# Kernel tuning notes

Measured on AMD Instinct MI355X. Metric: run time of the kernel, lower is better.

Reference implementation:

```python
import jax, jax.numpy as jnp
import numpy as np

# B videos, K topological sorts, N subtask nodes, S video segments, H = hsize
B, K, N, S, H = 8, 4, 16, 64, 512
NEG = -100.0  # torch.full((N,S), -100.0) init in dp_align


def setup_inputs() -> dict:
    key = jax.random.key(0)
    ks = jax.random.split(key, 6)
    return {
        "seg_text_feats": jax.random.normal(ks[0], (B, K, N, 2 * H), jnp.float32),
        "vid_feature": jax.random.normal(ks[1], (B, S, 2 * H), jnp.float32),
        "labels": jax.random.uniform(ks[2], (B,), jnp.float32),
        "W1": jax.random.normal(ks[3], (4 * H, H), jnp.float32) * 0.02,
        "b1": jnp.zeros((H,), jnp.float32),
        "w2": jax.random.normal(ks[4], (H,), jnp.float32) * 0.04,
        "b2": jnp.zeros((), jnp.float32),
    }


def _dp_single(logits):
    """Viterbi-style banded DP of dp_align for one (video, sort) pair.
    logits: [N, S]. Returns (best_score=arr[0,0], aggregated_logits, alignment[N]).
    Recurrence (faithful to the torch code):
      arr[n,s] = max(V_curr, arr[n,s+1]) where
        V_curr = logsig(logit[n,s])                     if n == N-1
        V_curr = logsig(logit[n,s]) + arr[n+1, s]       otherwise
      band: s in [n, S-N+n]; out-of-band cells stay -100.
    """
    n_nodes, n_segs = logits.shape
    L = jax.nn.log_sigmoid(logits)
    s_idx = jnp.arange(n_segs)

    def row_step(arr_next, xn):
        n, Ln = xn
        c = jnp.where(n == n_nodes - 1, Ln, Ln + arr_next)  # V_opt_curr per segment
        in_band = (s_idx >= n) & (s_idx <= n_segs - n_nodes + n)
        # arr[n,s] = max(max_{s'>=s in band} c[s'], -100)  (reverse cummax == seg loop)
        cm = jax.lax.cummax(jnp.where(in_band, c, -jnp.inf)[::-1])[::-1]
        row = jnp.where(in_band, jnp.maximum(cm, NEG), NEG)
        # choice[s]: took V_opt_curr (ties -> curr, matching >=); base case s=S-1 forced curr
        row_nxt = jnp.concatenate([row[1:], jnp.full((1,), -1e30, row.dtype)])
        choice = in_band & (c >= row_nxt)
        return row, (row, choice)

    arr0 = jnp.full((n_segs,), NEG, logits.dtype)
    xs = (jnp.arange(n_nodes - 1, -1, -1), L[::-1])  # nodes processed bottom-up
    _, (rows, choices) = jax.lax.scan(row_step, arr0, xs)
    best = rows[-1][0]          # arr[0, 0]
    choice = choices[::-1]      # reorder to ascending node index

    # Backpointer traceback: curr -> (node+1, seg+1) (record seg), next -> (node, seg+1)
    def step(state, _):
        node, seg, done, agg, align = state
        took = (~done) & choice[node, seg]
        agg = agg + jnp.where(took, logits[node, seg], 0.0)
        align = align.at[node].set(jnp.where(took, seg, align[node]))
        done = done | (took & (node == n_nodes - 1))
        node = jnp.where(took & (~done), node + 1, node)
        seg = jnp.where(done, seg, jnp.minimum(seg + 1, n_segs - 1))
        return (node, seg, done, agg, align), None

    init = (jnp.int32(0), jnp.int32(0), jnp.bool_(False),
            jnp.zeros((), logits.dtype), jnp.zeros((n_nodes,), jnp.int32))
    (_, _, _, agg, align), _ = jax.lax.scan(step, init, None, length=n_nodes + n_segs)
    return best, agg, align


def reference(seg_text_feats, vid_feature, labels, W1, b1, w2, b2):
    Bx, Kx, Nx, F2 = seg_text_feats.shape
    Sx = vid_feature.shape[1]
    # Batched query MLP over all (sort, node, segment) pairs (replaces the per-pair
    # batch-1 Linear+ReLU+Linear launches in the torch loop). Dropout(0.5) is eval-mode identity.
    t = jnp.broadcast_to(seg_text_feats[:, :, :, None, :], (Bx, Kx, Nx, Sx, F2))
    v = jnp.broadcast_to(vid_feature[:, None, None, :, :], (Bx, Kx, Nx, Sx, F2))
    cat = jnp.concatenate([t, v], axis=-1)                      # [B,K,N,S,4H]
    h1 = jax.nn.relu(jnp.einsum('bknsf,fh->bknsh', cat, W1) + b1)
    logits = jnp.einsum('bknsh,h->bkns', h1, w2) + b2           # [B,K,N,S]

    best, agg, align = jax.vmap(jax.vmap(_dp_single))(logits)   # [B,K], [B,K], [B,K,N]
    k = jnp.argmax(best, axis=-1)                               # best sort per video
    agg_b = jnp.take_along_axis(agg, k[:, None], axis=1)[:, 0]
    align_b = jnp.take_along_axis(align, k[:, None, None], axis=1)[:, 0]
    probs = jax.nn.sigmoid(agg_b)                               # ent_probs, [B]
    return probs, labels, align_b
```

## Files before the change

kernel.cpp:

```cpp
#include <hip/hip_runtime.h>
#include <math.h>

#define Bsz 8
#define Kc 4
#define Nn 16
#define Ss 64
#define Hh 512
#define F2 1024

__device__ __forceinline__ float logsigf(float x) {
    return fminf(x, 0.0f) - log1pf(expf(-fabsf(x)));
}

template<int Ctrl, int RowMask>
__device__ __forceinline__ float dpp_add(float x) {
    int v = __builtin_amdgcn_update_dpp(0, __float_as_int(x), Ctrl, RowMask, 0xf, false);
    return x + __int_as_float(v);
}
template<int Ctrl, int RowMask>
__device__ __forceinline__ float dpp_max(float x) {
    int v = __builtin_amdgcn_update_dpp(__float_as_int(-INFINITY), __float_as_int(x),
                                        Ctrl, RowMask, 0xf, false);
    return fmaxf(x, __int_as_float(v));
}
__device__ __forceinline__ float wave_scan_add(float x) {
    x = dpp_add<0x111, 0xf>(x);
    x = dpp_add<0x112, 0xf>(x);
    x = dpp_add<0x114, 0xf>(x);
    x = dpp_add<0x118, 0xf>(x);
    x = dpp_add<0x142, 0xa>(x);
    x = dpp_add<0x143, 0xc>(x);
    return x;
}
__device__ __forceinline__ float wave_scan_max(float x) {
    x = dpp_max<0x111, 0xf>(x);
    x = dpp_max<0x112, 0xf>(x);
    x = dpp_max<0x114, 0xf>(x);
    x = dpp_max<0x118, 0xf>(x);
    x = dpp_max<0x142, 0xa>(x);
    x = dpp_max<0x143, 0xc>(x);
    return x;
}

__global__ __launch_bounds__(512) void gemm_kernel(
    const float* __restrict__ seg, const float* __restrict__ vid,
    const float* __restrict__ W1,
    float* __restrict__ Tfin, float* __restrict__ Vfin)
{
    const int z = blockIdx.z;
    const float* __restrict__ Amat = z ? vid : seg;
    const float* __restrict__ Bmat = W1 + (z ? (size_t)F2 * Hh : 0);
    float* __restrict__ Out = z ? Vfin : Tfin;
    const int r0 = blockIdx.x * 64;
    const int n0 = blockIdx.y * 32;
    const int t = threadIdx.x;
    const int h   = t >> 8;
    const int tid = t & 255;

    __shared__ __align__(16) float As[2][2][32][68];
    __shared__ __align__(16) float Bs[2][2][32][36];

    const int mt = (tid >> 4) << 2;
    const int nt = (tid & 15) << 1;
    const int ar  = tid >> 3;
    const int ak4 = (tid & 7) << 2;
    const int bk  = tid >> 3;
    const int bc4 = (tid & 7) << 2;

    float4 ra0, ra1, rb0;
    auto load_step = [&](int s) {
        const int k0 = h * 512 + s * 32;
        ra0 = *reinterpret_cast<const float4*>(Amat + (size_t)(r0 + ar) * F2 + k0 + ak4);
        ra1 = *reinterpret_cast<const float4*>(Amat + (size_t)(r0 + ar + 32) * F2 + k0 + ak4);
        rb0 = *reinterpret_cast<const float4*>(Bmat + (size_t)(k0 + bk) * Hh + n0 + bc4);
    };
    auto write_step = [&](int buf) {
        As[h][buf][ak4 + 0][ar] = ra0.x; As[h][buf][ak4 + 1][ar] = ra0.y;
        As[h][buf][ak4 + 2][ar] = ra0.z; As[h][buf][ak4 + 3][ar] = ra0.w;
        As[h][buf][ak4 + 0][ar + 32] = ra1.x; As[h][buf][ak4 + 1][ar + 32] = ra1.y;
        As[h][buf][ak4 + 2][ar + 32] = ra1.z; As[h][buf][ak4 + 3][ar + 32] = ra1.w;
        *reinterpret_cast<float4*>(&Bs[h][buf][bk][bc4]) = rb0;
    };

    float acc[4][2] = {{0.f}};
    load_step(0);
    write_step(0);
    __syncthreads();
    #pragma unroll 1
    for (int s = 0; s < 16; ++s) {
        const int cur = s & 1;
        if (s + 1 < 16) load_step(s + 1);
        #pragma unroll
        for (int kk = 0; kk < 32; ++kk) {
            float4 a4 = *reinterpret_cast<const float4*>(&As[h][cur][kk][mt]);
            float2 b2 = *reinterpret_cast<const float2*>(&Bs[h][cur][kk][nt]);
            float av[4] = {a4.x, a4.y, a4.z, a4.w};
            #pragma unroll
            for (int i = 0; i < 4; ++i) {
                acc[i][0] = fmaf(av[i], b2.x, acc[i][0]);
                acc[i][1] = fmaf(av[i], b2.y, acc[i][1]);
            }
        }
        if (s + 1 < 16) {
            write_step(cur ^ 1);
            __syncthreads();
        }
    }
    __syncthreads();
    float* red = &As[0][0][0][0];
    if (h == 1) {
        #pragma unroll
        for (int i = 0; i < 4; ++i) {
            red[tid * 8 + i * 2 + 0] = acc[i][0];
            red[tid * 8 + i * 2 + 1] = acc[i][1];
        }
    }
    __syncthreads();
    if (h == 0) {
        #pragma unroll
        for (int i = 0; i < 4; ++i) {
            float2 o;
            o.x = acc[i][0] + red[tid * 8 + i * 2 + 0];
            o.y = acc[i][1] + red[tid * 8 + i * 2 + 1];
            *reinterpret_cast<float2*>(Out + (size_t)(r0 + mt + i) * Hh + n0 + nt) = o;
        }
    }
}

__global__ __launch_bounds__(256) void combine_kernel(
    const float* __restrict__ Tfin, const float* __restrict__ Vfin,
    const float* __restrict__ b1, const float* __restrict__ w2,
    const float* __restrict__ b2, float* __restrict__ logits)
{
    const int bid = blockIdx.x;
    const int b  = bid >> 5;
    const int sc = (bid >> 2) & 7;
    const int rq = bid & 3;
    const int t = threadIdx.x;
    const int wave = t >> 6, lane = t & 63;
    __shared__ float Vs[8][520];
    {
        const int s_l = t & 7;
        const int h0  = (t >> 3) << 4;
        const float* row = Vfin + (size_t)(b * Ss + sc * 8 + s_l) * Hh + h0;
        #pragma unroll
        for (int x4 = 0; x4 < 4; ++x4)
            *reinterpret_cast<float4*>(&Vs[s_l][h0 + 4 * x4]) =
                *reinterpret_cast<const float4*>(row + 4 * x4);
    }
    float w2r[8], b1r[8];
    #pragma unroll
    for (int j = 0; j < 8; ++j) { w2r[j] = w2[lane + 64 * j]; b1r[j] = b1[lane + 64 * j]; }
    const float bias2 = b2[0];
    __syncthreads();
    #pragma unroll
    for (int i = 0; i < 4; ++i) {
        const int kn = rq * 16 + wave * 4 + i;
        const int r  = b * 64 + kn;
        const float* trow = Tfin + (size_t)r * Hh;
        float tj[8];
        #pragma unroll
        for (int j = 0; j < 8; ++j) tj[j] = trow[lane + 64 * j] + b1r[j];
        #pragma unroll
        for (int s = 0; s < 8; ++s) {
            float sum = 0.f;
            #pragma unroll
            for (int j = 0; j < 8; ++j)
                sum = fmaf(fmaxf(tj[j] + Vs[s][lane + 64 * j], 0.f), w2r[j], sum);
            sum = wave_scan_add(sum);
            if (lane == 63) logits[(size_t)r * Ss + sc * 8 + s] = sum + bias2;
        }
    }
}

__global__ __launch_bounds__(256) void dp_kernel(
    const float* __restrict__ logits, const float* __restrict__ labels,
    float* __restrict__ out)
{
    const int b = blockIdx.x;
    const int t = threadIdx.x;
    const int k = t >> 6, rl = t & 63;
    const int sI = 63 - rl;
    __shared__ float lgs[Kc][Nn][Ss];
    __shared__ unsigned long long ch[Kc][Nn];
    __shared__ float bestS[Kc], aggS[Kc];
    __shared__ int alS[Kc][Nn];
    const float* lg = logits + (size_t)((b * Kc + k) * Nn) * Ss;
    float lv[Nn];
    #pragma unroll
    for (int n = 0; n < Nn; ++n) {
        lv[n] = lg[n * Ss + sI];
        lgs[k][n][sI] = lv[n];
    }
    float arr = -100.0f;
    #pragma unroll
    for (int n = Nn - 1; n >= 0; --n) {
        const float L = logsigf(lv[n]);
        const float c = (n == Nn - 1) ? L : (L + arr);
        const bool in_band = (rl <= 63 - n) && (rl >= 15 - n);
        float m = in_band ? c : -INFINITY;
        m = wave_scan_max(m);
        const float row = in_band ? fmaxf(m, -100.0f) : -100.0f;
        float rnA = __int_as_float(__builtin_amdgcn_update_dpp(
            __float_as_int(-1e30f), __float_as_int(row), 0x111, 0xf, 0xf, false));
        float b15 = __int_as_float(__builtin_amdgcn_update_dpp(
            0, __float_as_int(row), 0x142, 0xa, 0xf, false));
        float b31 = __int_as_float(__builtin_amdgcn_update_dpp(
            0, __float_as_int(row), 0x143, 0xc, 0xf, false));
        float rn = ((rl & 15) == 0 && rl != 0) ? ((rl == 32) ? b31 : b15) : rnA;
        unsigned long long mask = __ballot(in_band && (c >= rn));
        if (rl == 0) ch[k][n] = __brevll(mask);
        arr = row;
    }
    const float best = __shfl(arr, 63);
    __syncthreads();
    if (rl == 0) {
        float agg = 0.f;
        int start = 0;
        bool dead = false;
        int alignv[Nn];
        #pragma unroll
        for (int n = 0; n < Nn; ++n) {
            unsigned long long m2 = dead ? 0ull : (ch[k][n] & (~0ull << start));
            if (m2) {
                const int s = __builtin_ctzll(m2);
                agg += lgs[k][n][s];
                alignv[n] = s;
                start = s + 1;
            } else {
                alignv[n] = 0;
                dead = true;
            }
        }
        bestS[k] = best; aggS[k] = agg;
        #pragma unroll
        for (int n = 0; n < Nn; ++n) alS[k][n] = alignv[n];
    }
    __syncthreads();
    if (t == 0) {
        int kb = 0; float bb = bestS[0];
        #pragma unroll
        for (int kk = 1; kk < Kc; ++kk)
            if (bestS[kk] > bb) { bb = bestS[kk]; kb = kk; }
        out[b] = 1.0f / (1.0f + expf(-aggS[kb]));
        out[Bsz + b] = labels[b];
        #pragma unroll
        for (int n = 0; n < Nn; ++n)
            out[2 * Bsz + b * Nn + n] = (float)alS[kb][n];
    }
}

extern "C" void kernel_launch(void* const* d_in, const int* in_sizes, int n_in,
                              void* d_out, int out_size, void* d_ws, size_t ws_size,
                              hipStream_t stream) {
    const float* seg    = (const float*)d_in[0];
    const float* vid    = (const float*)d_in[1];
    const float* labels = (const float*)d_in[2];
    const float* W1     = (const float*)d_in[3];
    const float* b1     = (const float*)d_in[4];
    const float* w2     = (const float*)d_in[5];
    const float* b2     = (const float*)d_in[6];
    float* out = (float*)d_out;

    float* Tfin   = (float*)d_ws;
    float* Vfin   = Tfin + (size_t)512 * Hh;
    float* logits = Vfin + (size_t)512 * Hh;

    hipLaunchKernelGGL(gemm_kernel, dim3(8, 16, 2), dim3(512), 0, stream,
                       seg, vid, W1, Tfin, Vfin);
    hipLaunchKernelGGL(combine_kernel, dim3(256), dim3(256), 0, stream,
                       Tfin, Vfin, b1, w2, b2, logits);
    hipLaunchKernelGGL(dp_kernel, dim3(Bsz), dim3(256), 0, stream, logits, labels, out);
}
```

Baseline: 49.23 us.

## Fuse combine and DP into per-(video,sort) kernel with tiny finalize

Merges the logit-combine and Viterbi DP stages into one kernel with one block per (video, sort) pair, so logits stay in shared memory instead of going through global memory. A small finalize kernel then picks the best sort per video. The aim is to drop the global logits round trip and the DP kernel's 8-block serialization. The trade-off is that the combine work now runs on only 32 blocks instead of 256, which reduces parallelism for the heaviest stage.

```diff
diff --git a/kernel.cpp b/kernel.cpp
--- a/kernel.cpp
+++ b/kernel.cpp
@@ -127,72 +127,64 @@
     }
 }
 
-__global__ __launch_bounds__(256) void combine_kernel(
+__global__ __launch_bounds__(256) void combine_dp_kernel(
     const float* __restrict__ Tfin, const float* __restrict__ Vfin,
     const float* __restrict__ b1, const float* __restrict__ w2,
-    const float* __restrict__ b2, float* __restrict__ logits)
+    const float* __restrict__ b2, float* __restrict__ res)
 {
-    const int bid = blockIdx.x;
-    const int b  = bid >> 5;
-    const int sc = (bid >> 2) & 7;
-    const int rq = bid & 3;
+    const int blk = blockIdx.x;
+    const int b = blk >> 2;
     const int t = threadIdx.x;
     const int wave = t >> 6, lane = t & 63;
-    __shared__ float Vs[8][520];
-    {
-        const int s_l = t & 7;
-        const int h0  = (t >> 3) << 4;
-        const float* row = Vfin + (size_t)(b * Ss + sc * 8 + s_l) * Hh + h0;
-        #pragma unroll
-        for (int x4 = 0; x4 < 4; ++x4)
-            *reinterpret_cast<float4*>(&Vs[s_l][h0 + 4 * x4]) =
-                *reinterpret_cast<const float4*>(row + 4 * x4);
-    }
+    __shared__ float Vs[16][516];
+    __shared__ float lgs[Nn][Ss];
     float w2r[8], b1r[8];
     #pragma unroll
     for (int j = 0; j < 8; ++j) { w2r[j] = w2[lane + 64 * j]; b1r[j] = b1[lane + 64 * j]; }
     const float bias2 = b2[0];
-    __syncthreads();
-    #pragma unroll
-    for (int i = 0; i < 4; ++i) {
-        const int kn = rq * 16 + wave * 4 + i;
-        const int r  = b * 64 + kn;
+    float tj[4][8];
+    #pragma unroll
+    for (int n4 = 0; n4 < 4; ++n4) {
+        const int r = blk * Nn + wave * 4 + n4;
         const float* trow = Tfin + (size_t)r * Hh;
-        float tj[8];
-        #pragma unroll
-        for (int j = 0; j < 8; ++j) tj[j] = trow[lane + 64 * j] + b1r[j];
-        #pragma unroll
-        for (int s = 0; s < 8; ++s) {
-            float sum = 0.f;
+        #pragma unroll
+        for (int j = 0; j < 8; ++j) tj[n4][j] = trow[lane + 64 * j] + b1r[j];
+    }
+    #pragma unroll 1
+    for (int ch = 0; ch < 4; ++ch) {
+        __syncthreads();
+        {
+            const int s_l = t >> 4;
+            const int c0  = (t & 15) << 2;
+            const float* row = Vfin + (size_t)(b * Ss + ch * 16 + s_l) * Hh;
             #pragma unroll
-            for (int j = 0; j < 8; ++j)
-                sum = fmaf(fmaxf(tj[j] + Vs[s][lane + 64 * j], 0.f), w2r[j], sum);
-            sum = wave_scan_add(sum);
-            if (lane == 63) logits[(size_t)r * Ss + sc * 8 + s] = sum + bias2;
-        }
-    }
-}
-
-__global__ __launch_bounds__(256) void dp_kernel(
-    const float* __restrict__ logits, const float* __restrict__ labels,
-    float* __restrict__ out)
-{
-    const int b = blockIdx.x;
-    const int t = threadIdx.x;
-    const int k = t >> 6, rl = t & 63;
+            for (int x = 0; x < 8; ++x)
+                *reinterpret_cast<float4*>(&Vs[s_l][c0 + 64 * x]) =
+                    *reinterpret_cast<const float4*>(row + c0 + 64 * x);
+        }
+        __syncthreads();
+        #pragma unroll
+        for (int n4 = 0; n4 < 4; ++n4) {
+            #pragma unroll
+            for (int si = 0; si < 16; ++si) {
+                float sum = 0.f;
+                #pragma unroll
+                for (int j = 0; j < 8; ++j)
+                    sum = fmaf(fmaxf(tj[n4][j] + Vs[si][lane + 64 * j], 0.f), w2r[j], sum);
+                sum = wave_scan_add(sum);
+                if (lane == 63) lgs[wave * 4 + n4][ch * 16 + si] = sum + bias2;
+            }
+        }
+    }
+    __syncthreads();
+    if (wave != 0) return;
+    const int rl = lane;
     const int sI = 63 - rl;
-    __shared__ float lgs[Kc][Nn][Ss];
-    __shared__ unsigned long long ch[Kc][Nn];
-    __shared__ float bestS[Kc], aggS[Kc];
-    __shared__ int alS[Kc][Nn];
-    const float* lg = logits + (size_t)((b * Kc + k) * Nn) * Ss;
     float lv[Nn];
     #pragma unroll
-    for (int n = 0; n < Nn; ++n) {
-        lv[n] = lg[n * Ss + sI];
-        lgs[k][n][sI] = lv[n];
-    }
+    for (int n = 0; n < Nn; ++n) lv[n] = lgs[n][sI];
     float arr = -100.0f;
+    unsigned long long msk[Nn];
     #pragma unroll
     for (int n = Nn - 1; n >= 0; --n) {
         const float L = logsigf(lv[n]);
@@ -209,44 +201,55 @@
             0, __float_as_int(row), 0x143, 0xc, 0xf, false));
         float rn = ((rl & 15) == 0 && rl != 0) ? ((rl == 32) ? b31 : b15) : rnA;
         unsigned long long mask = __ballot(in_band && (c >= rn));
-        if (rl == 0) ch[k][n] = __brevll(mask);
+        msk[n] = __brevll(mask);
         arr = row;
     }
     const float best = __shfl(arr, 63);
-    __syncthreads();
+    float agg = 0.f;
+    int start = 0;
+    bool dead = false;
+    int alignv[Nn];
+    #pragma unroll
+    for (int n = 0; n < Nn; ++n) {
+        unsigned long long m2 = dead ? 0ull : (msk[n] & (~0ull << start));
+        if (m2) {
+            const int s = __builtin_ctzll(m2);
+            agg += __shfl(lv[n], 63 - s);
+            alignv[n] = s;
+            start = s + 1;
+        } else {
+            alignv[n] = 0;
+            dead = true;
+        }
+    }
     if (rl == 0) {
-        float agg = 0.f;
-        int start = 0;
-        bool dead = false;
-        int alignv[Nn];
-        #pragma unroll
-        for (int n = 0; n < Nn; ++n) {
-            unsigned long long m2 = dead ? 0ull : (ch[k][n] & (~0ull << start));
-            if (m2) {
-                const int s = __builtin_ctzll(m2);
-                agg += lgs[k][n][s];
-                alignv[n] = s;
-                start = s + 1;
-            } else {
-                alignv[n] = 0;
-                dead = true;
-            }
-        }
-        bestS[k] = best; aggS[k] = agg;
-        #pragma unroll
-        for (int n = 0; n < Nn; ++n) alS[k][n] = alignv[n];
-    }
-    __syncthreads();
-    if (t == 0) {
-        int kb = 0; float bb = bestS[0];
-        #pragma unroll
-        for (int kk = 1; kk < Kc; ++kk)
-            if (bestS[kk] > bb) { bb = bestS[kk]; kb = kk; }
-        out[b] = 1.0f / (1.0f + expf(-aggS[kb]));
-        out[Bsz + b] = labels[b];
+        float* rr = res + blk * 20;
+        rr[0] = best;
+        rr[1] = agg;
+        #pragma unroll
+        for (int n = 0; n < Nn; ++n) rr[2 + n] = (float)alignv[n];
+    }
+}
+
+__global__ __launch_bounds__(64) void finalize_kernel(
+    const float* __restrict__ res, const float* __restrict__ labels,
+    float* __restrict__ out)
+{
+    const int t = threadIdx.x;
+    if (t < Bsz) {
+        int kb = 0;
+        float bb = res[(t * 4 + 0) * 20];
+        #pragma unroll
+        for (int kk = 1; kk < Kc; ++kk) {
+            float v = res[(t * 4 + kk) * 20];
+            if (v > bb) { bb = v; kb = kk; }
+        }
+        const float* rr = res + (t * 4 + kb) * 20;
+        out[t] = 1.0f / (1.0f + expf(-rr[1]));
+        out[Bsz + t] = labels[t];
         #pragma unroll
         for (int n = 0; n < Nn; ++n)
-            out[2 * Bsz + b * Nn + n] = (float)alS[kb][n];
+            out[2 * Bsz + t * Nn + n] = rr[2 + n];
     }
 }
 
@@ -262,13 +265,14 @@
     const float* b2     = (const float*)d_in[6];
     float* out = (float*)d_out;
 
-    float* Tfin   = (float*)d_ws;
-    float* Vfin   = Tfin + (size_t)512 * Hh;
-    float* logits = Vfin + (size_t)512 * Hh;
+    float* Tfin = (float*)d_ws;
+    float* Vfin = Tfin + (size_t)512 * Hh;
+    float* res  = Vfin + (size_t)512 * Hh;
 
     hipLaunchKernelGGL(gemm_kernel, dim3(8, 16, 2), dim3(512), 0, stream,
                        seg, vid, W1, Tfin, Vfin);
-    hipLaunchKernelGGL(combine_kernel, dim3(256), dim3(256), 0, stream,
-                       Tfin, Vfin, b1, w2, b2, logits);
-    hipLaunchKernelGGL(dp_kernel, dim3(Bsz), dim3(256), 0, stream, logits, labels, out);
-}
+    hipLaunchKernelGGL(combine_dp_kernel, dim3(32), dim3(256), 0, stream,
+                       Tfin, Vfin, b1, w2, b2, res);
+    hipLaunchKernelGGL(finalize_kernel, dim3(1), dim3(64), 0, stream,
+                       res, labels, out);
+}
```

Result: slower. 71.46 us (+45.1%).

## Split GEMM K across four groups with 4x4 register tiles; widen combine grid

Applied to the files above, without the earlier changes.

The GEMM now uses four 128-thread groups, each covering a quarter of K with a 4x4 register tile per thread instead of a 4x2 tile, and reduces the partial sums through shared memory. The aim is more FMAs per shared-memory load and fewer serial K steps per block. The combine kernel doubles its grid, gives each wave two rows that share every V load, and uses coalesced V staging, which adds parallelism and reuse. The cost is a larger shared-memory footprint and a heavier three-way reduction at the end of the GEMM.

```diff
diff --git a/kernel.cpp b/kernel.cpp
--- a/kernel.cpp
+++ b/kernel.cpp
@@ -24,21 +24,15 @@
     return fmaxf(x, __int_as_float(v));
 }
 __device__ __forceinline__ float wave_scan_add(float x) {
-    x = dpp_add<0x111, 0xf>(x);
-    x = dpp_add<0x112, 0xf>(x);
-    x = dpp_add<0x114, 0xf>(x);
-    x = dpp_add<0x118, 0xf>(x);
-    x = dpp_add<0x142, 0xa>(x);
-    x = dpp_add<0x143, 0xc>(x);
+    x = dpp_add<0x111, 0xf>(x); x = dpp_add<0x112, 0xf>(x);
+    x = dpp_add<0x114, 0xf>(x); x = dpp_add<0x118, 0xf>(x);
+    x = dpp_add<0x142, 0xa>(x); x = dpp_add<0x143, 0xc>(x);
     return x;
 }
 __device__ __forceinline__ float wave_scan_max(float x) {
-    x = dpp_max<0x111, 0xf>(x);
-    x = dpp_max<0x112, 0xf>(x);
-    x = dpp_max<0x114, 0xf>(x);
-    x = dpp_max<0x118, 0xf>(x);
-    x = dpp_max<0x142, 0xa>(x);
-    x = dpp_max<0x143, 0xc>(x);
+    x = dpp_max<0x111, 0xf>(x); x = dpp_max<0x112, 0xf>(x);
+    x = dpp_max<0x114, 0xf>(x); x = dpp_max<0x118, 0xf>(x);
+    x = dpp_max<0x142, 0xa>(x); x = dpp_max<0x143, 0xc>(x);
     return x;
 }
 
@@ -54,75 +48,93 @@
     const int r0 = blockIdx.x * 64;
     const int n0 = blockIdx.y * 32;
     const int t = threadIdx.x;
-    const int h   = t >> 8;
-    const int tid = t & 255;
-
-    __shared__ __align__(16) float As[2][2][32][68];
-    __shared__ __align__(16) float Bs[2][2][32][36];
-
-    const int mt = (tid >> 4) << 2;
-    const int nt = (tid & 15) << 1;
-    const int ar  = tid >> 3;
-    const int ak4 = (tid & 7) << 2;
-    const int bk  = tid >> 3;
-    const int bc4 = (tid & 7) << 2;
-
-    float4 ra0, ra1, rb0;
+    const int q   = t >> 7;
+    const int qt  = t & 127;
+
+    __shared__ __align__(16) float As[4][2][32][68];
+    __shared__ __align__(16) float Bs[4][2][32][36];
+
+    const int mt = (qt >> 3) << 2;
+    const int nt = (qt & 7) << 2;
+    const int ari = qt >> 1;
+    const int aq0 = (qt & 1) << 2;
+    const int brk = qt >> 2;
+    const int bcb = (qt & 3) << 3;
+
+    float4 ra0, ra1, ra2, ra3, rb0, rb1;
     auto load_step = [&](int s) {
-        const int k0 = h * 512 + s * 32;
-        ra0 = *reinterpret_cast<const float4*>(Amat + (size_t)(r0 + ar) * F2 + k0 + ak4);
-        ra1 = *reinterpret_cast<const float4*>(Amat + (size_t)(r0 + ar + 32) * F2 + k0 + ak4);
-        rb0 = *reinterpret_cast<const float4*>(Bmat + (size_t)(k0 + bk) * Hh + n0 + bc4);
+        const int k0 = q * 256 + s * 32;
+        const float* arow = Amat + (size_t)(r0 + ari) * F2 + k0;
+        ra0 = *reinterpret_cast<const float4*>(arow + 4 * (aq0 + 0));
+        ra1 = *reinterpret_cast<const float4*>(arow + 4 * (aq0 + 1));
+        ra2 = *reinterpret_cast<const float4*>(arow + 4 * (aq0 + 2));
+        ra3 = *reinterpret_cast<const float4*>(arow + 4 * (aq0 + 3));
+        const float* brow = Bmat + (size_t)(k0 + brk) * Hh + n0 + bcb;
+        rb0 = *reinterpret_cast<const float4*>(brow);
+        rb1 = *reinterpret_cast<const float4*>(brow + 4);
     };
     auto write_step = [&](int buf) {
-        As[h][buf][ak4 + 0][ar] = ra0.x; As[h][buf][ak4 + 1][ar] = ra0.y;
-        As[h][buf][ak4 + 2][ar] = ra0.z; As[h][buf][ak4 + 3][ar] = ra0.w;
-        As[h][buf][ak4 + 0][ar + 32] = ra1.x; As[h][buf][ak4 + 1][ar + 32] = ra1.y;
-        As[h][buf][ak4 + 2][ar + 32] = ra1.z; As[h][buf][ak4 + 3][ar + 32] = ra1.w;
-        *reinterpret_cast<float4*>(&Bs[h][buf][bk][bc4]) = rb0;
+        As[q][buf][4*(aq0+0)+0][ari] = ra0.x; As[q][buf][4*(aq0+0)+1][ari] = ra0.y;
+        As[q][buf][4*(aq0+0)+2][ari] = ra0.z; As[q][buf][4*(aq0+0)+3][ari] = ra0.w;
+        As[q][buf][4*(aq0+1)+0][ari] = ra1.x; As[q][buf][4*(aq0+1)+1][ari] = ra1.y;
+        As[q][buf][4*(aq0+1)+2][ari] = ra1.z; As[q][buf][4*(aq0+1)+3][ari] = ra1.w;
+        As[q][buf][4*(aq0+2)+0][ari] = ra2.x; As[q][buf][4*(aq0+2)+1][ari] = ra2.y;
+        As[q][buf][4*(aq0+2)+2][ari] = ra2.z; As[q][buf][4*(aq0+2)+3][ari] = ra2.w;
+        As[q][buf][4*(aq0+3)+0][ari] = ra3.x; As[q][buf][4*(aq0+3)+1][ari] = ra3.y;
+        As[q][buf][4*(aq0+3)+2][ari] = ra3.z; As[q][buf][4*(aq0+3)+3][ari] = ra3.w;
+        *reinterpret_cast<float4*>(&Bs[q][buf][brk][bcb])     = rb0;
+        *reinterpret_cast<float4*>(&Bs[q][buf][brk][bcb + 4]) = rb1;
     };
 
-    float acc[4][2] = {{0.f}};
+    float acc[4][4] = {{0.f}};
+    auto compute = [&](int cur) {
+        #pragma unroll
+        for (int kk = 0; kk < 32; ++kk) {
+            float4 a4 = *reinterpret_cast<const float4*>(&As[q][cur][kk][mt]);
+            float4 b4 = *reinterpret_cast<const float4*>(&Bs[q][cur][kk][nt]);
+            float av[4] = {a4.x, a4.y, a4.z, a4.w};
+            float bv[4] = {b4.x, b4.y, b4.z, b4.w};
+            #pragma unroll
+            for (int i = 0; i < 4; ++i)
+                #pragma unroll
+                for (int j = 0; j < 4; ++j)
+                    acc[i][j] = fmaf(av[i], bv[j], acc[i][j]);
+        }
+    };
+
     load_step(0);
     write_step(0);
     __syncthreads();
     #pragma unroll 1
-    for (int s = 0; s < 16; ++s) {
+    for (int s = 0; s < 8; ++s) {
         const int cur = s & 1;
-        if (s + 1 < 16) load_step(s + 1);
-        #pragma unroll
-        for (int kk = 0; kk < 32; ++kk) {
-            float4 a4 = *reinterpret_cast<const float4*>(&As[h][cur][kk][mt]);
-            float2 b2 = *reinterpret_cast<const float2*>(&Bs[h][cur][kk][nt]);
-            float av[4] = {a4.x, a4.y, a4.z, a4.w};
-            #pragma unroll
-            for (int i = 0; i < 4; ++i) {
-                acc[i][0] = fmaf(av[i], b2.x, acc[i][0]);
-                acc[i][1] = fmaf(av[i], b2.y, acc[i][1]);
-            }
-        }
-        if (s + 1 < 16) {
+        if (s + 1 < 8) load_step(s + 1);
+        compute(cur);
+        if (s + 1 < 8) {
             write_step(cur ^ 1);
             __syncthreads();
         }
     }
     __syncthreads();
     float* red = &As[0][0][0][0];
-    if (h == 1) {
+    if (q >= 1) {
+        #pragma unroll
+        for (int i = 0; i < 4; ++i)
+            *reinterpret_cast<float4*>(&red[(((q - 1) * 128 + qt) * 16) + 4 * i]) =
+                make_float4(acc[i][0], acc[i][1], acc[i][2], acc[i][3]);
+    }
+    __syncthreads();
+    if (q == 0) {
         #pragma unroll
         for (int i = 0; i < 4; ++i) {
-            red[tid * 8 + i * 2 + 0] = acc[i][0];
-            red[tid * 8 + i * 2 + 1] = acc[i][1];
-        }
-    }
-    __syncthreads();
-    if (h == 0) {
-        #pragma unroll
-        for (int i = 0; i < 4; ++i) {
-            float2 o;
-            o.x = acc[i][0] + red[tid * 8 + i * 2 + 0];
-            o.y = acc[i][1] + red[tid * 8 + i * 2 + 1];
-            *reinterpret_cast<float2*>(Out + (size_t)(r0 + mt + i) * Hh + n0 + nt) = o;
+            float4 o = make_float4(acc[i][0], acc[i][1], acc[i][2], acc[i][3]);
+            #pragma unroll
+            for (int p = 0; p < 3; ++p) {
+                float4 v = *reinterpret_cast<const float4*>(
+                    &red[((p * 128 + qt) * 16) + 4 * i]);
+                o.x += v.x; o.y += v.y; o.z += v.z; o.w += v.w;
+            }
+            *reinterpret_cast<float4*>(Out + (size_t)(r0 + mt + i) * Hh + n0 + nt) = o;
         }
     }
 }
@@ -133,42 +145,52 @@
     const float* __restrict__ b2, float* __restrict__ logits)
 {
     const int bid = blockIdx.x;
-    const int b  = bid >> 5;
-    const int sc = (bid >> 2) & 7;
-    const int rq = bid & 3;
+    const int b  = bid >> 6;
+    const int sc = (bid >> 3) & 7;
+    const int rq = bid & 7;
     const int t = threadIdx.x;
     const int wave = t >> 6, lane = t & 63;
-    __shared__ float Vs[8][520];
+    __shared__ float Vs[8][516];
     {
-        const int s_l = t & 7;
-        const int h0  = (t >> 3) << 4;
-        const float* row = Vfin + (size_t)(b * Ss + sc * 8 + s_l) * Hh + h0;
-        #pragma unroll
-        for (int x4 = 0; x4 < 4; ++x4)
-            *reinterpret_cast<float4*>(&Vs[s_l][h0 + 4 * x4]) =
-                *reinterpret_cast<const float4*>(row + 4 * x4);
+        const int row = t >> 5;
+        const int f0  = t & 31;
+        const float* src = Vfin + (size_t)(b * Ss + sc * 8 + row) * Hh;
+        #pragma unroll
+        for (int j = 0; j < 4; ++j)
+            *reinterpret_cast<float4*>(&Vs[row][(f0 + 32 * j) * 4]) =
+                *reinterpret_cast<const float4*>(src + (f0 + 32 * j) * 4);
     }
     float w2r[8], b1r[8];
     #pragma unroll
     for (int j = 0; j < 8; ++j) { w2r[j] = w2[lane + 64 * j]; b1r[j] = b1[lane + 64 * j]; }
     const float bias2 = b2[0];
-    __syncthreads();
-    #pragma unroll
-    for (int i = 0; i < 4; ++i) {
-        const int kn = rq * 16 + wave * 4 + i;
-        const int r  = b * 64 + kn;
-        const float* trow = Tfin + (size_t)r * Hh;
-        float tj[8];
-        #pragma unroll
-        for (int j = 0; j < 8; ++j) tj[j] = trow[lane + 64 * j] + b1r[j];
-        #pragma unroll
-        for (int s = 0; s < 8; ++s) {
-            float sum = 0.f;
-            #pragma unroll
-            for (int j = 0; j < 8; ++j)
-                sum = fmaf(fmaxf(tj[j] + Vs[s][lane + 64 * j], 0.f), w2r[j], sum);
-            sum = wave_scan_add(sum);
-            if (lane == 63) logits[(size_t)r * Ss + sc * 8 + s] = sum + bias2;
+    float tj0[8], tj1[8];
+    {
+        const int r0i = b * 64 + rq * 8 + wave * 2;
+        const float* t0 = Tfin + (size_t)r0i * Hh;
+        const float* t1 = t0 + Hh;
+        #pragma unroll
+        for (int j = 0; j < 8; ++j) {
+            tj0[j] = t0[lane + 64 * j] + b1r[j];
+            tj1[j] = t1[lane + 64 * j] + b1r[j];
+        }
+    }
+    __syncthreads();
+    const int rbase = b * 64 + rq * 8 + wave * 2;
+    #pragma unroll
+    for (int si = 0; si < 8; ++si) {
+        float s0 = 0.f, s1 = 0.f;
+        #pragma unroll
+        for (int j = 0; j < 8; ++j) {
+            const float v = Vs[si][lane + 64 * j];
+            s0 = fmaf(fmaxf(tj0[j] + v, 0.f), w2r[j], s0);
+            s1 = fmaf(fmaxf(tj1[j] + v, 0.f), w2r[j], s1);
+        }
+        s0 = wave_scan_add(s0);
+        s1 = wave_scan_add(s1);
+        if (lane == 63) {
+            logits[(size_t)rbase * Ss + sc * 8 + si]       = s0 + bias2;
+            logits[(size_t)(rbase + 1) * Ss + sc * 8 + si] = s1 + bias2;
         }
     }
 }
@@ -268,7 +290,7 @@
 
     hipLaunchKernelGGL(gemm_kernel, dim3(8, 16, 2), dim3(512), 0, stream,
                        seg, vid, W1, Tfin, Vfin);
-    hipLaunchKernelGGL(combine_kernel, dim3(256), dim3(256), 0, stream,
+    hipLaunchKernelGGL(combine_kernel, dim3(512), dim3(256), 0, stream,
                        Tfin, Vfin, b1, w2, b2, logits);
     hipLaunchKernelGGL(dp_kernel, dim3(Bsz), dim3(256), 0, stream, logits, labels, out);
 }
```

Result: slower. 98.80 us (+100.7%).
